# Kernel tuning notes

Measured on AMD Instinct MI355X. Metric: run time of the kernel, lower is better.

The kernel has to match this reference:

```python
import jax, jax.numpy as jnp
import numpy as np

PI = 3.1415927410125732
N = 4096
L = 1.28e-3          # box side [m]
VEL = 5e-7
RC = 3.15e-6         # Rc = diameter/2
RR = 8e-6
RO = 2.5e-5
RA = np.inf
DT_TRANS = 1.4e-14   # DT (translational diffusion)
DR = 0.0028
GAMMA = 25.0
DT = 0.2             # timestep dt
COLL_ITERS = 30      # fixed cap for collision-resolution do-while (orig caps at 1000)


def setup_inputs() -> dict:
    key = jax.random.key(0)
    ks = jax.random.split(key, 7)
    pos_re = jax.random.uniform(ks[0], (N,), jnp.float32) * L
    pos_im = jax.random.uniform(ks[1], (N,), jnp.float32) * L
    ang = jax.random.uniform(ks[2], (N,), jnp.float32, -PI, PI)
    ori_re = jnp.cos(ang)
    ori_im = jnp.sin(ang)
    deltas = jax.random.uniform(ks[3], (N,), jnp.float32) * 0.5
    rot_noise = jax.random.normal(ks[4], (N,), jnp.float32)
    tn_re = jax.random.normal(ks[5], (N,), jnp.float32)
    tn_im = jax.random.normal(ks[6], (N,), jnp.float32)
    return {"pos_re": pos_re, "pos_im": pos_im, "ori_re": ori_re, "ori_im": ori_im,
            "deltas": deltas, "rot_noise": rot_noise, "tn_re": tn_re, "tn_im": tn_im}


def _wrap(diff):
    # torch get_anglediff wrap: (-2pi,2pi) -> ~(-pi,pi)
    diff = jnp.where(diff <= -PI, jnp.mod(diff, PI), diff)
    return diff - (diff >= PI).astype(diff.dtype) * (2.0 * PI)


def _anglediff(a, b):
    return _wrap(jnp.angle(a) - jnp.angle(b))


def _cossim(a, b):
    # nn.CosineSimilarity(dim=1, eps=1e-14) on view_as_real vectors
    dot = a.real * b.real + a.imag * b.imag
    na = jnp.maximum(jnp.abs(a), 1e-14)
    nb = jnp.maximum(jnp.abs(b), 1e-14)
    return dot / (na * nb)


def _mvc(W, z):
    # real [n,n] mask @ complex [n] vector
    return W @ z.real + 1j * (W @ z.imag)


def _solve_collisions(pos):
    n = pos.shape[0]
    eye_f = jnp.eye(n, dtype=jnp.float32)
    eye_c = eye_f.astype(pos.dtype)

    def step(p):
        diff = p[None, :] - p[:, None] + eye_c  # [i,j] = pos_j - pos_i; diag dummy 1 (nan-safe)
        absd = jnp.abs(diff)
        coll = absd <= (2.0 * RC - eye_f)       # diag threshold negative -> self excluded
        move = jnp.where(coll, diff / jnp.where(coll, absd, 1.0) * ((2.1 * RC - absd) * 0.5), 0.0)
        return p - move.sum(axis=1), coll.sum()

    def body(carry, _):
        p, cont = carry
        p_new, ncoll = step(p)
        p = jnp.where(cont, p_new, p)           # do-while: apply move, then continue if collisions
        return (p, jnp.logical_and(cont, ncoll > 0)), None

    body = jax.checkpoint(body)
    (pos, _), _ = jax.lax.scan(body, (pos, jnp.array(True)), None, length=COLL_ITERS)
    return pos


def _forward(pos_re, pos_im, ori_re, ori_im, deltas, rot_noise, tn_re, tn_im):
    pos = (pos_re + 1j * pos_im).astype(jnp.complex64)
    ori = (ori_re + 1j * ori_im).astype(jnp.complex64)
    n = pos.shape[0]
    eye_b = jnp.eye(n, dtype=bool)

    # pairwise |pos_i - pos_j|; diag made 1 to keep abs() grad-safe (diag is masked out / re-added below)
    dists = jnp.abs(pos[:, None] - pos[None, :] + jnp.eye(n, dtype=pos.dtype))
    mask_rr = (dists <= RR) & ~eye_b              # repulsion zone, self excluded (eye subtracted in orig)
    mask_ro = (dists <= RO + RC) | eye_b          # orientation zone, self included (diag dist 0 in orig)
    mask_ra = (dists <= RA + RC) | eye_b          # Ra = inf -> all ones

    # alpha == 2*pi exactly -> within_view branch skipped (matches original)
    ang = jnp.angle(ori)
    abs_ad = jnp.abs(_wrap(ang[:, None] - ang[None, :]))
    in_front = abs_ad < PI / 2

    Wrr = (mask_rr & in_front).astype(jnp.float32)
    Wro = mask_ro.astype(jnp.float32)
    Wra = mask_ra.astype(jnp.float32)

    n_r = Wrr.sum(axis=1)
    S = _mvc(Wrr, pos) / jnp.maximum(n_r, 1.0) - pos * jnp.sign(n_r)
    d = -S

    n_a = Wra.sum(axis=1)
    cms = _mvc(Wra, pos) / jnp.maximum(n_a, 1.0)
    Ps = cms - pos * jnp.sign(n_a)

    osum = _mvc(Wro, ori)
    left = Ps * jnp.exp(1j * deltas)
    right = Ps * jnp.exp(-1j * deltas)

    # T (=300) >= T_release (=200): choose best turn by cosine similarity
    best = jnp.where(_cossim(left, osum) >= _cossim(right, osum), left, right)

    has_rep = jnp.abs(d) > 0.0
    d_safe = jnp.where(has_rep, d, jnp.ones_like(d))
    att = jnp.where(has_rep, _anglediff(d_safe, ori), _anglediff(best, ori))

    s2dr = np.float32(np.sqrt(2.0 * DR))
    sdt = np.float32(np.sqrt(DT))
    rot = jnp.exp(1j * (DT * GAMMA * DR * jnp.sin(att) + rot_noise * s2dr * sdt))

    # complex standard normal: real/imag each N(0, 1/sqrt(2))
    tnoise = (tn_re + 1j * tn_im) * np.float32(np.sqrt(0.5)) * np.float32(np.sqrt(2.0 * DT_TRANS))
    trans = DT * VEL * ori + tnoise * sdt

    new_pos = _solve_collisions(pos + trans)
    new_ori = ori * rot

    c2r = lambda z: jnp.stack([z.real, z.imag], axis=-1)
    # [5, N, 2]: positions, orientations, orientation_sums, leftturns, rightturns (real views)
    return jnp.stack([c2r(new_pos), c2r(new_ori), c2r(osum), c2r(left), c2r(right)], axis=0)


def reference(pos_re, pos_im, ori_re, ori_im, deltas, rot_noise, tn_re, tn_im):
    return _forward(pos_re, pos_im, ori_re, ori_im, deltas, rot_noise, tn_re, tn_im)
```

## Files before the change

kernel.cpp:

```cpp
#include <hip/hip_runtime.h>

#define NPART 4096
#define PI_F 3.1415927410125732f
#define TWO_PI_F 6.2831854820251465f
#define SENT 4096

__device__ __forceinline__ float wrapf(float d) {
    if (d <= -PI_F) {
        d = fmodf(d, PI_F);
        if (d < 0.0f) d += PI_F;
    }
    if (d >= PI_F) d -= TWO_PI_F;
    return d;
}

__global__ __launch_bounds__(512)
void k_interact(const float* __restrict__ pr, const float* __restrict__ pim,
                const float* __restrict__ orr, const float* __restrict__ oim,
                const float* __restrict__ deltas,
                const float* __restrict__ rot_noise,
                const float* __restrict__ tn_re, const float* __restrict__ tn_im,
                float* __restrict__ out,
                uint2* __restrict__ recQuad, int* __restrict__ recC,
                unsigned short* __restrict__ recNbr16) {
    constexpr float RR_F  = 8e-6f;
    constexpr float RR2   = RR_F * RR_F;
    constexpr float ROC_F = (float)(2.5e-5 + 3.15e-6);
    constexpr float ROC2  = ROC_F * ROC_F;
    constexpr float CUT_F = 14.3e-6f;
    constexpr float CUT2  = CUT_F * CUT_F;

    __shared__ float2 lsP[512];
    __shared__ float2 lsO[512];
    __shared__ float rA0[512], rA1[512], rA2[512], rA3[512], rA4[512];
    __shared__ float rB0[512], rB1[512], rB2[512], rB3[512], rB4[512];
    __shared__ float cr_[512], ci_[512];
    __shared__ int ncnt[16];
    __shared__ unsigned short nbrL[16 * 16];

    int tid = threadIdx.x;
    int li = tid & 7, sl = tid >> 3;
    int i0 = blockIdx.x * 16 + li;
    int i1 = i0 + 8;

    if (tid < 16) ncnt[tid] = 0;

    float pxA = pr[i0], pyA = pim[i0], oxA = orr[i0], oyA = oim[i0];
    float pxB = pr[i1], pyB = pim[i1], oxB = orr[i1], oyB = oim[i1];

    float nAr = 0.0f, SAre = 0.0f, SAim = 0.0f, oAre = 0.0f, oAim = 0.0f;
    float nBr = 0.0f, SBre = 0.0f, SBim = 0.0f, oBre = 0.0f, oBim = 0.0f;
    float cs_re = 0.0f, cs_im = 0.0f;

    for (int c = 0; c < 8; ++c) {
        int j0 = c * 512;
        __syncthreads();
        float jr = pr[j0 + tid], ji = pim[j0 + tid];
        lsP[tid] = make_float2(jr, ji);
        lsO[tid] = make_float2(orr[j0 + tid], oim[j0 + tid]);
        cs_re += jr; cs_im += ji;
        __syncthreads();
#pragma unroll
        for (int t = 0; t < 8; ++t) {
            int jj = sl * 8 + ((t + sl) & 7);
            int j = j0 + jj;
            float2 pv = lsP[jj];
            float drA = pxA - pv.x, diA = pyA - pv.y;
            float d2A = drA * drA + diA * diA;
            float drB = pxB - pv.x, diB = pyB - pv.y;
            float d2B = drB * drB + diB * diB;
            if (__any((d2A <= ROC2) | (d2B <= ROC2))) {
                float2 ov = lsO[jj];
                if (d2A <= ROC2) { oAre += ov.x; oAim += ov.y; }
                float dotA = oxA * ov.x + oyA * ov.y;
                if ((d2A <= RR2) & (dotA > 0.0f) & (j != i0)) {
                    nAr += 1.0f; SAre += pv.x; SAim += pv.y;
                }
                if (d2A <= CUT2 && j != i0) {
                    int slot = atomicAdd(&ncnt[li], 1);
                    if (slot < 16) nbrL[li * 16 + slot] = (unsigned short)j;
                }
                if (d2B <= ROC2) { oBre += ov.x; oBim += ov.y; }
                float dotB = oxB * ov.x + oyB * ov.y;
                if ((d2B <= RR2) & (dotB > 0.0f) & (j != i1)) {
                    nBr += 1.0f; SBre += pv.x; SBim += pv.y;
                }
                if (d2B <= CUT2 && j != i1) {
                    int slot = atomicAdd(&ncnt[li + 8], 1);
                    if (slot < 16) nbrL[(li + 8) * 16 + slot] = (unsigned short)j;
                }
            }
        }
    }

    rA0[tid] = nAr; rA1[tid] = SAre; rA2[tid] = SAim; rA3[tid] = oAre; rA4[tid] = oAim;
    rB0[tid] = nBr; rB1[tid] = SBre; rB2[tid] = SBim; rB3[tid] = oBre; rB4[tid] = oBim;
    cr_[tid] = cs_re; ci_[tid] = cs_im;
    __syncthreads();
    for (int s = 256; s >= 8; s >>= 1) {
        if (tid < s) {
            rA0[tid] += rA0[tid + s]; rA1[tid] += rA1[tid + s];
            rA2[tid] += rA2[tid + s]; rA3[tid] += rA3[tid + s];
            rA4[tid] += rA4[tid + s];
            rB0[tid] += rB0[tid + s]; rB1[tid] += rB1[tid + s];
            rB2[tid] += rB2[tid + s]; rB3[tid] += rB3[tid + s];
            rB4[tid] += rB4[tid + s];
            cr_[tid] += cr_[tid + s];  ci_[tid] += ci_[tid + s];
        }
        __syncthreads();
    }
    if (tid < 4) { cr_[tid] += cr_[tid + 4]; ci_[tid] += ci_[tid + 4]; }
    __syncthreads();
    if (tid < 2) { cr_[tid] += cr_[tid + 2]; ci_[tid] += ci_[tid + 2]; }
    __syncthreads();
    if (tid == 0) { cr_[0] += cr_[1]; ci_[0] += ci_[1]; }
    __syncthreads();

    if (tid < 16) {
        int i = blockIdx.x * 16 + tid;
        float n_r, S_re, S_im, o_re, o_im, px, py, ox, oy;
        if (tid < 8) {
            n_r = rA0[tid]; S_re = rA1[tid]; S_im = rA2[tid];
            o_re = rA3[tid]; o_im = rA4[tid];
            px = pxA; py = pyA; ox = oxA; oy = oyA;
        } else {
            int g = tid - 8;
            n_r = rB0[g]; S_re = rB1[g]; S_im = rB2[g];
            o_re = rB3[g]; o_im = rB4[g];
            px = pxB; py = pyB; ox = oxB; oy = oyB;
        }

        float maxnr = fmaxf(n_r, 1.0f);
        float sgn = (n_r > 0.0f) ? 1.0f : 0.0f;
        float Sre = S_re / maxnr - px * sgn;
        float Sim = S_im / maxnr - py * sgn;
        float d_re = -Sre, d_im = -Sim;

        float cmsx = cr_[0] * (1.0f / 4096.0f);
        float cmsy = ci_[0] * (1.0f / 4096.0f);
        float Ps_re = cmsx - px;
        float Ps_im = cmsy - py;

        float dl = deltas[i];
        float cd = cosf(dl), sd = sinf(dl);
        float l_re = Ps_re * cd - Ps_im * sd;
        float l_im = Ps_re * sd + Ps_im * cd;
        float r_re = Ps_re * cd + Ps_im * sd;
        float r_im = Ps_im * cd - Ps_re * sd;

        float nb   = fmaxf(hypotf(o_re, o_im), 1e-14f);
        float na_l = fmaxf(hypotf(l_re, l_im), 1e-14f);
        float na_r = fmaxf(hypotf(r_re, r_im), 1e-14f);
        float csl = (l_re * o_re + l_im * o_im) / (na_l * nb);
        float csr = (r_re * o_re + r_im * o_im) / (na_r * nb);
        float b_re = (csl >= csr) ? l_re : r_re;
        float b_im = (csl >= csr) ? l_im : r_im;

        float ai = atan2f(oy, ox);
        bool has_rep = (d_re != 0.0f) || (d_im != 0.0f);
        float att;
        if (has_rep) att = wrapf(atan2f(d_im, d_re) - ai);
        else         att = wrapf(atan2f(b_im, b_re) - ai);

        constexpr float GDD  = (float)(0.2 * 25.0 * 0.0028);
        constexpr float S2DR = 0.07483314773547883f;
        constexpr float SDT  = 0.44721359549995793f;
        float theta = GDD * sinf(att) + (rot_noise[i] * S2DR) * SDT;
        float rr_ = cosf(theta), ri_ = sinf(theta);

        float no_re = ox * rr_ - oy * ri_;
        float no_im = ox * ri_ + oy * rr_;

        constexpr float DTVEL = (float)(0.2 * 5e-7);
        constexpr float C1 = 0.70710678118654752f;
        constexpr float C2 = 1.6733200530681511e-07f;
        float t_re = DTVEL * ox + ((tn_re[i] * C1) * C2) * SDT;
        float t_im = DTVEL * oy + ((tn_im[i] * C1) * C2) * SDT;
        float p0x = px + t_re, p0y = py + t_im;

        float2* o2 = (float2*)out;
        o2[i]            = make_float2(p0x, p0y);
        o2[1 * 4096 + i] = make_float2(no_re, no_im);
        o2[2 * 4096 + i] = make_float2(o_re, o_im);
        o2[3 * 4096 + i] = make_float2(l_re, l_im);
        o2[4 * 4096 + i] = make_float2(r_re, r_im);

        int c = min(ncnt[tid], 16);
        unsigned q0 = (c > 0) ? nbrL[tid * 16 + 0] : (unsigned)SENT;
        unsigned q1 = (c > 1) ? nbrL[tid * 16 + 1] : (unsigned)SENT;
        unsigned q2 = (c > 2) ? nbrL[tid * 16 + 2] : (unsigned)SENT;
        unsigned q3 = (c > 3) ? nbrL[tid * 16 + 3] : (unsigned)SENT;
        recQuad[i] = make_uint2(q0 | (q1 << 16), q2 | (q3 << 16));
        recC[i] = c;
        if (c > 4) {
            int cp = (c + 3) & ~3;
            for (int m = 4; m < cp; ++m)
                recNbr16[i * 16 + m] = (m < c) ? nbrL[tid * 16 + m]
                                               : (unsigned short)SENT;
        }
    }
}

__global__ __launch_bounds__(1024)
void k_coll_all(const uint2* __restrict__ recQuad, const int* __restrict__ recC,
                const unsigned short* __restrict__ recNbr16,
                float* __restrict__ out) {
    constexpr float TWO_RC  = (float)(2.0 * 3.15e-6);
    constexpr float TWO_RC2 = TWO_RC * TWO_RC;
    constexpr float C21RC   = (float)(2.1 * 3.15e-6);

    __shared__ float2 pos[NPART + 2];
    __shared__ __align__(16) unsigned short pool[128 * 16];
    __shared__ int flg[2];
    __shared__ int poolCnt;
    __shared__ unsigned bmp[2][132];

    int tid = threadIdx.x;
    if (tid == 0) {
        pos[SENT] = make_float2(1e9f, 1e9f);
        flg[0] = 0; flg[1] = 0; poolCnt = 0;
    }
    if (tid < 132) { bmp[0][tid] = 0u; bmp[1][tid] = 0u; }

    const float2* o2in = (const float2*)out;
    float myx[4], myy[4];
    int myc[4], myo[4];
    int nq0[4], nq1[4], nq2[4], nq3[4];
    bool pm[4];
#pragma unroll
    for (int s = 0; s < 4; ++s) {
        int i = s * 1024 + tid;
        float2 p = o2in[i];
        myx[s] = p.x; myy[s] = p.y;
        pos[i] = p;
        uint2 q = recQuad[i];
        nq0[s] = q.x & 0xffff; nq1[s] = q.x >> 16;
        nq2[s] = q.y & 0xffff; nq3[s] = q.y >> 16;
        myc[s] = recC[i];
        myo[s] = -1;
        pm[s] = true;
    }
    __syncthreads();

#pragma unroll
    for (int s = 0; s < 4; ++s) {
        if (myc[s] > 4) {
            int r = atomicAdd(&poolCnt, 1);
            if (r < 128) {
                int i = s * 1024 + tid;
                const uint4* src = (const uint4*)&recNbr16[i * 16];
                uint4* dst = (uint4*)&pool[r * 16];
                dst[0] = src[0]; dst[1] = src[1];
                myo[s] = r;
            }
        }
    }
    __syncthreads();

    for (int it = 0; it < 30; ++it) {
        int cur = it & 1, nxt = cur ^ 1;
        if (tid < 132) bmp[nxt][tid] = 0u;

        float nx[4], ny[4];
        int ncs[4];
#pragma unroll
        for (int s = 0; s < 4; ++s) {
            ncs[s] = 0;
            int c = myc[s];
            if (c > 0) {
                bool dirty;
                if (it == 0 || c > 4) {
                    dirty = true;
                } else {
                    unsigned hit = pm[s] ? 1u : 0u;
                    hit |= (bmp[cur][nq0[s] >> 5] >> (nq0[s] & 31)) & 1u;
                    hit |= (bmp[cur][nq1[s] >> 5] >> (nq1[s] & 31)) & 1u;
                    hit |= (bmp[cur][nq2[s] >> 5] >> (nq2[s] & 31)) & 1u;
                    hit |= (bmp[cur][nq3[s] >> 5] >> (nq3[s] & 31)) & 1u;
                    dirty = hit != 0u;
                }
                if (dirty) {
                    float px = myx[s], py = myy[s];
                    float mre = 0.0f, mim = 0.0f;
                    int nc = 0;
                    float2 q0 = pos[nq0[s]], q1 = pos[nq1[s]];
                    float2 q2 = pos[nq2[s]], q3 = pos[nq3[s]];
#define COLL_ONE(q)                                                     \
                    {                                                   \
                        float dr = (q).x - px, di = (q).y - py;         \
                        float d2 = dr * dr + di * di;                   \
                        if (d2 <= TWO_RC2) {                            \
                            float a = sqrtf(d2);                        \
                            float mm = (C21RC - a) * 0.5f / a;          \
                            mre += dr * mm; mim += di * mm; ++nc;       \
                        }                                               \
                    }
                    COLL_ONE(q0) COLL_ONE(q1) COLL_ONE(q2) COLL_ONE(q3)
                    for (int m0 = 4; m0 < c; m0 += 4) {
                        uint2 w;
                        if (myo[s] >= 0)
                            w = *(const uint2*)&pool[myo[s] * 16 + m0];
                        else
                            w = *(const uint2*)&recNbr16[(s * 1024 + tid) * 16 + m0];
                        int j0 = w.x & 0xffff, j1 = w.x >> 16;
                        int j2 = w.y & 0xffff, j3 = w.y >> 16;
                        float2 t0 = pos[j0], t1 = pos[j1], t2 = pos[j2], t3 = pos[j3];
                        COLL_ONE(t0) COLL_ONE(t1) COLL_ONE(t2) COLL_ONE(t3)
                    }
#undef COLL_ONE
                    ncs[s] = nc;
                    nx[s] = px - mre; ny[s] = py - mim;
                }
            }
        }
        __syncthreads();
#pragma unroll
        for (int s = 0; s < 4; ++s) {
            pm[s] = (ncs[s] > 0);
            if (ncs[s] > 0) {
                int i = s * 1024 + tid;
                myx[s] = nx[s]; myy[s] = ny[s];
                pos[i] = make_float2(nx[s], ny[s]);
                atomicOr(&bmp[nxt][i >> 5], 1u << (i & 31));
            }
        }
        int any = ncs[0] | ncs[1] | ncs[2] | ncs[3];
        if (any) flg[it & 1] = 1;
        if (tid == 0) flg[(it + 1) & 1] = 0;
        __syncthreads();
        if (flg[it & 1] == 0) break;
    }

    float2* o2 = (float2*)out;
#pragma unroll
    for (int s = 0; s < 4; ++s)
        o2[s * 1024 + tid] = make_float2(myx[s], myy[s]);
}

extern "C" void kernel_launch(void* const* d_in, const int* in_sizes, int n_in,
                              void* d_out, int out_size, void* d_ws, size_t ws_size,
                              hipStream_t stream) {
    const float* pos_re = (const float*)d_in[0];
    const float* pos_im = (const float*)d_in[1];
    const float* ori_re = (const float*)d_in[2];
    const float* ori_im = (const float*)d_in[3];
    const float* deltas = (const float*)d_in[4];
    const float* rot_noise = (const float*)d_in[5];
    const float* tn_re = (const float*)d_in[6];
    const float* tn_im = (const float*)d_in[7];
    float* out = (float*)d_out;

    uint2* recQuad = (uint2*)d_ws;
    int* recC = (int*)(recQuad + NPART);
    unsigned short* recNbr16 = (unsigned short*)(recC + NPART);

    k_interact<<<256, 512, 0, stream>>>(pos_re, pos_im, ori_re, ori_im,
                                        deltas, rot_noise, tn_re, tn_im,
                                        out, recQuad, recC, recNbr16);
    k_coll_all<<<1, 1024, 0, stream>>>(recQuad, recC, recNbr16, out);
}
```

Baseline: 120.1 us.

## Fuse collision solver into interaction kernel via last-block-done atomic counter

Merges the two kernels into one: every block does the interaction work, then bumps a global atomic counter, and the last block to finish runs the collision-resolution loop with 512 threads, each handling 8 particles. This removes a kernel launch and the gap between the two kernels. In exchange it adds a memset launch, threadfence-based ordering, and a collision phase with half the threads. The larger static shared-memory footprint of the fused kernel may also reduce occupancy in the interaction phase.

```diff
diff --git a/kernel.cpp b/kernel.cpp
--- a/kernel.cpp
+++ b/kernel.cpp
@@ -15,14 +15,14 @@
 }
 
 __global__ __launch_bounds__(512)
-void k_interact(const float* __restrict__ pr, const float* __restrict__ pim,
-                const float* __restrict__ orr, const float* __restrict__ oim,
-                const float* __restrict__ deltas,
-                const float* __restrict__ rot_noise,
-                const float* __restrict__ tn_re, const float* __restrict__ tn_im,
-                float* __restrict__ out,
-                uint2* __restrict__ recQuad, int* __restrict__ recC,
-                unsigned short* __restrict__ recNbr16) {
+void k_fused(const float* __restrict__ pr, const float* __restrict__ pim,
+             const float* __restrict__ orr, const float* __restrict__ oim,
+             const float* __restrict__ deltas,
+             const float* __restrict__ rot_noise,
+             const float* __restrict__ tn_re, const float* __restrict__ tn_im,
+             float* __restrict__ out,
+             uint2* __restrict__ recQuad, int* __restrict__ recC,
+             unsigned short* __restrict__ recNbr16, int* __restrict__ gcnt) {
     constexpr float RR_F  = 8e-6f;
     constexpr float RR2   = RR_F * RR_F;
     constexpr float ROC_F = (float)(2.5e-5 + 3.15e-6);
@@ -37,6 +37,12 @@
     __shared__ float cr_[512], ci_[512];
     __shared__ int ncnt[16];
     __shared__ unsigned short nbrL[16 * 16];
+    __shared__ float2 pos[NPART + 2];
+    __shared__ __align__(16) unsigned short pool[128 * 16];
+    __shared__ int flg[2];
+    __shared__ int poolCnt;
+    __shared__ unsigned bmp[2][132];
+    __shared__ int lastFlag;
 
     int tid = threadIdx.x;
     int li = tid & 7, sl = tid >> 3;
@@ -199,23 +205,21 @@
                                                : (unsigned short)SENT;
         }
     }
-}
-
-__global__ __launch_bounds__(1024)
-void k_coll_all(const uint2* __restrict__ recQuad, const int* __restrict__ recC,
-                const unsigned short* __restrict__ recNbr16,
-                float* __restrict__ out) {
+
+    __syncthreads();
+    if (tid == 0) {
+        __threadfence();
+        unsigned t = atomicAdd((unsigned*)gcnt, 1u);
+        lastFlag = (t == 255u);
+    }
+    __syncthreads();
+    if (!lastFlag) return;
+    __threadfence();
+
     constexpr float TWO_RC  = (float)(2.0 * 3.15e-6);
     constexpr float TWO_RC2 = TWO_RC * TWO_RC;
     constexpr float C21RC   = (float)(2.1 * 3.15e-6);
 
-    __shared__ float2 pos[NPART + 2];
-    __shared__ __align__(16) unsigned short pool[128 * 16];
-    __shared__ int flg[2];
-    __shared__ int poolCnt;
-    __shared__ unsigned bmp[2][132];
-
-    int tid = threadIdx.x;
     if (tid == 0) {
         pos[SENT] = make_float2(1e9f, 1e9f);
         flg[0] = 0; flg[1] = 0; poolCnt = 0;
@@ -223,13 +227,13 @@
     if (tid < 132) { bmp[0][tid] = 0u; bmp[1][tid] = 0u; }
 
     const float2* o2in = (const float2*)out;
-    float myx[4], myy[4];
-    int myc[4], myo[4];
-    int nq0[4], nq1[4], nq2[4], nq3[4];
-    bool pm[4];
-#pragma unroll
-    for (int s = 0; s < 4; ++s) {
-        int i = s * 1024 + tid;
+    float myx[8], myy[8];
+    int myc[8], myo[8];
+    int nq0[8], nq1[8], nq2[8], nq3[8];
+    bool pm[8];
+#pragma unroll
+    for (int s = 0; s < 8; ++s) {
+        int i = s * 512 + tid;
         float2 p = o2in[i];
         myx[s] = p.x; myy[s] = p.y;
         pos[i] = p;
@@ -243,11 +247,11 @@
     __syncthreads();
 
 #pragma unroll
-    for (int s = 0; s < 4; ++s) {
+    for (int s = 0; s < 8; ++s) {
         if (myc[s] > 4) {
             int r = atomicAdd(&poolCnt, 1);
             if (r < 128) {
-                int i = s * 1024 + tid;
+                int i = s * 512 + tid;
                 const uint4* src = (const uint4*)&recNbr16[i * 16];
                 uint4* dst = (uint4*)&pool[r * 16];
                 dst[0] = src[0]; dst[1] = src[1];
@@ -261,10 +265,10 @@
         int cur = it & 1, nxt = cur ^ 1;
         if (tid < 132) bmp[nxt][tid] = 0u;
 
-        float nx[4], ny[4];
-        int ncs[4];
-#pragma unroll
-        for (int s = 0; s < 4; ++s) {
+        float nx[8], ny[8];
+        int ncs[8];
+#pragma unroll
+        for (int s = 0; s < 8; ++s) {
             ncs[s] = 0;
             int c = myc[s];
             if (c > 0) {
@@ -301,7 +305,7 @@
                         if (myo[s] >= 0)
                             w = *(const uint2*)&pool[myo[s] * 16 + m0];
                         else
-                            w = *(const uint2*)&recNbr16[(s * 1024 + tid) * 16 + m0];
+                            w = *(const uint2*)&recNbr16[(s * 512 + tid) * 16 + m0];
                         int j0 = w.x & 0xffff, j1 = w.x >> 16;
                         int j2 = w.y & 0xffff, j3 = w.y >> 16;
                         float2 t0 = pos[j0], t1 = pos[j1], t2 = pos[j2], t3 = pos[j3];
@@ -314,17 +318,18 @@
             }
         }
         __syncthreads();
-#pragma unroll
-        for (int s = 0; s < 4; ++s) {
+        int any = 0;
+#pragma unroll
+        for (int s = 0; s < 8; ++s) {
             pm[s] = (ncs[s] > 0);
             if (ncs[s] > 0) {
-                int i = s * 1024 + tid;
+                int i = s * 512 + tid;
                 myx[s] = nx[s]; myy[s] = ny[s];
                 pos[i] = make_float2(nx[s], ny[s]);
                 atomicOr(&bmp[nxt][i >> 5], 1u << (i & 31));
             }
-        }
-        int any = ncs[0] | ncs[1] | ncs[2] | ncs[3];
+            any |= ncs[s];
+        }
         if (any) flg[it & 1] = 1;
         if (tid == 0) flg[(it + 1) & 1] = 0;
         __syncthreads();
@@ -333,8 +338,8 @@
 
     float2* o2 = (float2*)out;
 #pragma unroll
-    for (int s = 0; s < 4; ++s)
-        o2[s * 1024 + tid] = make_float2(myx[s], myy[s]);
+    for (int s = 0; s < 8; ++s)
+        o2[s * 512 + tid] = make_float2(myx[s], myy[s]);
 }
 
 extern "C" void kernel_launch(void* const* d_in, const int* in_sizes, int n_in,
@@ -350,12 +355,13 @@
     const float* tn_im = (const float*)d_in[7];
     float* out = (float*)d_out;
 
-    uint2* recQuad = (uint2*)d_ws;
+    int* gcnt = (int*)d_ws;
+    uint2* recQuad = (uint2*)((char*)d_ws + 16);
     int* recC = (int*)(recQuad + NPART);
     unsigned short* recNbr16 = (unsigned short*)(recC + NPART);
 
-    k_interact<<<256, 512, 0, stream>>>(pos_re, pos_im, ori_re, ori_im,
-                                        deltas, rot_noise, tn_re, tn_im,
-                                        out, recQuad, recC, recNbr16);
-    k_coll_all<<<1, 1024, 0, stream>>>(recQuad, recC, recNbr16, out);
+    hipMemsetAsync(gcnt, 0, 16, stream);
+    k_fused<<<256, 512, 0, stream>>>(pos_re, pos_im, ori_re, ori_im,
+                                     deltas, rot_noise, tn_re, tn_im,
+                                     out, recQuad, recC, recNbr16, gcnt);
 }
```

Result: slower. 145.0 us (+20.7%).
